# Kernel tuning notes

Hardware: AMD Instinct MI355X
Metric: run time of the kernel (lower is better)

Reference implementation:

```python
import jax, jax.numpy as jnp
import numpy as np

NUM_HEADS = 16

def setup_inputs() -> dict:
    key = jax.random.key(0)
    ks = jax.random.split(key, 7)
    B, N, D = 2, 2048, 1024
    x = jax.random.normal(ks[0], (B, N, D), dtype=jnp.float32)
    gamma = jax.random.uniform(ks[1], (B, NUM_HEADS), dtype=jnp.float32)
    dist_matrix = jax.random.uniform(ks[2], (N, N), dtype=jnp.float32)
    W_qkv = jax.random.normal(ks[3], (D, 3 * D), dtype=jnp.float32) * (D ** -0.5)
    b_qkv = jnp.zeros((3 * D,), dtype=jnp.float32)
    W_proj = jax.random.normal(ks[4], (D, D), dtype=jnp.float32) * (D ** -0.5)
    b_proj = jnp.zeros((D,), dtype=jnp.float32)
    return {"x": x, "gamma": gamma, "dist_matrix": dist_matrix,
            "W_qkv": W_qkv, "b_qkv": b_qkv, "W_proj": W_proj, "b_proj": b_proj}

def reference(x, gamma, dist_matrix, W_qkv, b_qkv, W_proj, b_proj):
    B, N, D = x.shape
    H = NUM_HEADS
    hd = D // H
    scale = D ** -0.5  # standard_scale=False -> dim**-0.5
    # qkv projection: [B,N,3D] -> [3,B,H,N,hd]
    qkv = (x @ W_qkv + b_qkv).reshape(B, N, 3, H, hd).transpose(2, 0, 3, 1, 4)
    q, k, v = qkv[0], qkv[1], qkv[2]
    # scores with zoom bias: [B,H,N,N]
    scores = jnp.einsum('bhnd,bhmd->bhnm', q, k) * scale
    scores = scores - gamma[:, :, None, None] * dist_matrix[None, None, :, :]
    attn = jax.nn.softmax(scores, axis=-1)
    out = jnp.einsum('bhnm,bhmd->bhnd', attn, v)  # [B,H,N,hd]
    out = out.transpose(0, 2, 1, 3).reshape(B, N, D)
    return out @ W_proj + b_proj
```

## Files before the change

### kernel.cpp

```cpp
#include <hip/hip_runtime.h>
#include <cstdint>
#include <cstddef>

#define HD 64
#define NH 16
#define BATCH 2
#define SEQ 2048
#define DIM 1024
#define SCALE 0.03125f
#define LOG2E 1.4426950408889634f
#define QSCALE (SCALE * LOG2E)
#define NT (SEQ / 64)
#define SOFF 16.0f

typedef short bf16x8 __attribute__((ext_vector_type(8)));
typedef float f32x4 __attribute__((ext_vector_type(4)));
typedef unsigned u32x2 __attribute__((ext_vector_type(2)));
typedef unsigned u32x4 __attribute__((ext_vector_type(4)));

#define GL16(gp, lp) __builtin_amdgcn_global_load_lds( \
    (const __attribute__((address_space(1))) unsigned int*)(gp), \
    (__attribute__((address_space(3))) unsigned int*)(lp), 16, 0, 0)

static __device__ __forceinline__ unsigned short f2bf(float f) {
  union { float f; unsigned u; } a; a.f = f;
  unsigned r = a.u + 0x7fffu + ((a.u >> 16) & 1u);
  return (unsigned short)(r >> 16);
}

static __device__ __forceinline__ f32x4 zero4() {
  f32x4 z; z[0] = 0.f; z[1] = 0.f; z[2] = 0.f; z[3] = 0.f; return z;
}

__global__ void convert_x(const float* __restrict__ in, unsigned short* __restrict__ out, int n4) {
  int i = blockIdx.x * blockDim.x + threadIdx.x;
  if (i < n4) {
    float4 v = reinterpret_cast<const float4*>(in)[i];
    ushort4 o;
    o.x = f2bf(v.x); o.y = f2bf(v.y); o.z = f2bf(v.z); o.w = f2bf(v.w);
    reinterpret_cast<ushort4*>(out)[i] = o;
  }
}

__global__ void transpose_convert(const float* __restrict__ in, unsigned short* __restrict__ out,
                                  int R, int C) {
  __shared__ float tile[32][33];
  int bx = blockIdx.x * 32;
  int by = blockIdx.y * 32;
  int tx = threadIdx.x, ty = threadIdx.y;
  #pragma unroll
  for (int i = 0; i < 32; i += 8)
    tile[ty + i][tx] = in[(size_t)(by + ty + i) * C + bx + tx];
  __syncthreads();
  #pragma unroll
  for (int i = 0; i < 32; i += 8)
    out[(size_t)(bx + ty + i) * R + by + tx] = f2bf(tile[tx][ty + i]);
}

__global__ __launch_bounds__(256) void gemm128(
    const unsigned short* __restrict__ A, const unsigned short* __restrict__ Bt,
    const float* __restrict__ bias, int K, int mode,
    unsigned short* __restrict__ qo, unsigned short* __restrict__ ko,
    unsigned short* __restrict__ vo, float* __restrict__ outf) {
  __shared__ __attribute__((aligned(16))) unsigned short As[128 * 64];
  __shared__ __attribute__((aligned(16))) unsigned short Bs[128 * 64];
  const int tid = threadIdx.x;
  const int lane = tid & 63, w = tid >> 6;
  const int lo = lane & 15, hi = lane >> 4;
  const int wm = w >> 1, wn = w & 1;
  const int gx = gridDim.x;
  const int nwg = gx * gridDim.y;
  const int flat = blockIdx.y * gx + blockIdx.x;
  const int swz = (flat & 7) * (nwg >> 3) + (flat >> 3);
  const int m0 = (swz / gx) * 128, n0 = (swz % gx) * 128;
  const int srow = tid >> 3, scol = (tid & 7) * 8;
  const unsigned short* abase = A + (size_t)(m0 + srow) * K + scol;
  const unsigned short* bbase = Bt + (size_t)(n0 + srow) * K + scol;

  f32x4 acc[4][4];
  #pragma unroll
  for (int mr = 0; mr < 4; ++mr)
    #pragma unroll
    for (int nr = 0; nr < 4; ++nr) acc[mr][nr] = zero4();

  const int nkt = K / 64;
  for (int kt = 0; kt < nkt; ++kt) {
    const unsigned short* ak = abase + kt * 64;
    const unsigned short* bk = bbase + kt * 64;
    #pragma unroll
    for (int i = 0; i < 4; ++i) {
      GL16(ak + (size_t)(32 * i) * K, &As[(w * 64 + 256 * i) * 8]);
      GL16(bk + (size_t)(32 * i) * K, &Bs[(w * 64 + 256 * i) * 8]);
    }
    __syncthreads();
    __builtin_amdgcn_s_setprio(1);
    #pragma unroll
    for (int kc = 0; kc < 2; ++kc) {
      bf16x8 af[4], bfr[4];
      #pragma unroll
      for (int mr = 0; mr < 4; ++mr)
        af[mr] = *reinterpret_cast<const bf16x8*>(
            &As[(wm * 64 + mr * 16 + lo) * 64 + kc * 32 + hi * 8]);
      #pragma unroll
      for (int nr = 0; nr < 4; ++nr)
        bfr[nr] = *reinterpret_cast<const bf16x8*>(
            &Bs[(wn * 64 + nr * 16 + lo) * 64 + kc * 32 + hi * 8]);
      #pragma unroll
      for (int mr = 0; mr < 4; ++mr)
        #pragma unroll
        for (int nr = 0; nr < 4; ++nr)
          acc[mr][nr] = __builtin_amdgcn_mfma_f32_16x16x32_bf16(af[mr], bfr[nr], acc[mr][nr], 0, 0, 0);
    }
    __builtin_amdgcn_s_setprio(0);
    __syncthreads();
  }

  #pragma unroll
  for (int nr = 0; nr < 4; ++nr) {
    const int gcol = n0 + wn * 64 + nr * 16 + lo;
    const float bv = bias[gcol];
    #pragma unroll
    for (int mr = 0; mr < 4; ++mr)
      #pragma unroll
      for (int j = 0; j < 4; ++j) {
        const int grow = m0 + wm * 64 + mr * 16 + hi * 4 + j;
        float val = acc[mr][nr][j] + bv;
        if (mode == 0) {
          int which = gcol >> 10;
          int hh = (gcol >> 6) & 15;
          int d = gcol & 63;
          int bb = grow >> 11;
          int n = grow & 2047;
          if (which == 0) {
            qo[((size_t)(bb * NH + hh) * SEQ + n) * HD + d] = f2bf(val * QSCALE);
          } else if (which == 1) {
            ko[((size_t)(bb * NH + hh) * SEQ + n) * HD + d] = f2bf(val);
          } else {
            vo[((size_t)(bb * NH + hh) * HD + d) * SEQ + n] = f2bf(val);
          }
        } else {
          outf[(size_t)grow * DIM + gcol] = val;
        }
      }
  }
}

__global__ __launch_bounds__(256, 4) void attn_kernel(
    const unsigned short* __restrict__ qb, const unsigned short* __restrict__ kb,
    const unsigned short* __restrict__ vtb, const float* __restrict__ gamma,
    const float* __restrict__ dist, unsigned short* __restrict__ ab) {
  __shared__ __attribute__((aligned(16))) unsigned short Ks[2][64 * 64];
  __shared__ __attribute__((aligned(16))) unsigned short Vt[2][64 * 64];
  __shared__ __attribute__((aligned(16))) unsigned short Ps[4 * 16 * 64];
  const int tid = threadIdx.x;
  const int lane = tid & 63;
  const int w = tid >> 6;
  const int lo = lane & 15;
  const int hi = lane >> 4;
  const int idx = blockIdx.x;
  const int bh = idx & 31;
  const int qt = idx >> 5;
  const int b = bh >> 4, h = bh & 15;
  const int qrow0 = qt * 64 + w * 16;
  const float g2 = gamma[bh] * LOG2E;

  const size_t base = (size_t)bh * SEQ * HD;
  const size_t vtbase = (size_t)bh * HD * SEQ;

  bf16x8 qf[2];
  #pragma unroll
  for (int kc = 0; kc < 2; ++kc)
    qf[kc] = *reinterpret_cast<const bf16x8*>(
        &qb[base + (size_t)(qrow0 + lo) * HD + kc * 32 + hi * 8]);

  const float* drow = dist + (size_t)(qrow0 + lo) * SEQ + hi * 4;

  f32x4 o[4];
  #pragma unroll
  for (int db = 0; db < 4; ++db) o[db] = zero4();
  float l_run = 0.f;

  const int srow = tid >> 3;
  const int schunk = (tid & 7) ^ (srow & 7);
  const unsigned short* ksrc0 = kb + base + (size_t)srow * HD + schunk * 8;
  const unsigned short* ksrc1 = ksrc0 + (size_t)32 * HD;
  const unsigned short* vsrc0 = vtb + vtbase + (size_t)srow * SEQ + schunk * 8;
  const unsigned short* vsrc1 = vsrc0 + (size_t)32 * SEQ;

  unsigned short* const psw = &Ps[w * 1024 + lo * 64];

  GL16(ksrc0, &Ks[0][w * 512]);
  GL16(ksrc1, &Ks[0][2048 + w * 512]);
  GL16(vsrc0, &Vt[0][w * 512]);
  GL16(vsrc1, &Vt[0][2048 + w * 512]);

#define ITER(T, CUR)                                                                   \
  {                                                                                    \
                                \
    asm volatile("s_waitcnt vmcnt(2)" ::: "memory");                                   \
    __builtin_amdgcn_s_barrier();                                                      \
                      \
    f32x4 dv[4];                                                                       \
    { const float* dp = drow + (T) * 64;                                               \
      _Pragma("unroll")                                                                \
      for (int nb = 0; nb < 4; ++nb)                                                   \
        dv[nb] = *reinterpret_cast<const f32x4*>(dp + nb * 16);                        \
    }                                                                                  \
    __builtin_amdgcn_sched_barrier(0);                                                 \
                                                                  \
    if ((T) + 1 < NT) {                                                                \
      const size_t m1 = (size_t)((T) + 1) * 64;                                        \
      GL16(ksrc0 + m1 * HD, &Ks[(CUR) ^ 1][w * 512]);                                  \
      GL16(ksrc1 + m1 * HD, &Ks[(CUR) ^ 1][2048 + w * 512]);                           \
    }                                                                                  \
    __builtin_amdgcn_sched_barrier(0);                                                 \
                                                         \
    f32x4 s[4];                                                                        \
    _Pragma("unroll")                                                                  \
    for (int nb = 0; nb < 4; ++nb) {                                                   \
      s[nb][0] = -SOFF; s[nb][1] = -SOFF; s[nb][2] = -SOFF; s[nb][3] = -SOFF;          \
    }                                                                                  \
    __builtin_amdgcn_s_setprio(1);                                                     \
    _Pragma("unroll")                                                                  \
    for (int nb = 0; nb < 4; ++nb)                                                     \
      _Pragma("unroll")                                                                \
      for (int kc = 0; kc < 2; ++kc) {                                                 \
        bf16x8 kf = *reinterpret_cast<const bf16x8*>(                                  \
            &Ks[CUR][(nb * 16 + lo) * 64 + ((kc * 4 + hi) ^ (lo & 7)) * 8]);           \
        s[nb] = __builtin_amdgcn_mfma_f32_16x16x32_bf16(kf, qf[kc], s[nb], 0, 0, 0);   \
      }                                                                                \
    __builtin_amdgcn_s_setprio(0);                                                     \
                         \
    float psum = 0.f;                                                                  \
    _Pragma("unroll")                                                                  \
    for (int nb = 0; nb < 4; ++nb) {                                                   \
      float p0 = exp2f(__builtin_fmaf(-g2, dv[nb][0], s[nb][0]));                      \
      float p1 = exp2f(__builtin_fmaf(-g2, dv[nb][1], s[nb][1]));                      \
      float p2 = exp2f(__builtin_fmaf(-g2, dv[nb][2], s[nb][2]));                      \
      float p3 = exp2f(__builtin_fmaf(-g2, dv[nb][3], s[nb][3]));                      \
      psum += (p0 + p1) + (p2 + p3);                                                   \
      unsigned pk0, pk1;                                                               \
      asm("v_cvt_pk_bf16_f32 %0, %1, %2" : "=v"(pk0) : "v"(p0), "v"(p1));              \
      asm("v_cvt_pk_bf16_f32 %0, %1, %2" : "=v"(pk1) : "v"(p2), "v"(p3));              \
      u32x2 pw_; pw_[0] = pk0; pw_[1] = pk1;                                           \
      *reinterpret_cast<u32x2*>(&psw[(((nb << 2) + hi) ^ lo) * 4]) = pw_;              \
    }                                                                                  \
    psum += __shfl_xor(psum, 16, 64);                                                  \
    psum += __shfl_xor(psum, 32, 64);                                                  \
    l_run += psum;                                                                     \
                  \
    if ((T) + 1 < NT)                                                                  \
      asm volatile("s_waitcnt vmcnt(2)" ::: "memory");                                 \
    else                                                                               \
      asm volatile("s_waitcnt vmcnt(0)" ::: "memory");                                 \
    __builtin_amdgcn_s_barrier();                                                      \
                                                                  \
    if ((T) + 1 < NT) {                                                                \
      const int m1 = ((T) + 1) * 64;                                                   \
      GL16(vsrc0 + m1, &Vt[(CUR) ^ 1][w * 512]);                                       \
      GL16(vsrc1 + m1, &Vt[(CUR) ^ 1][2048 + w * 512]);                                \
    }                                                                                  \
    __builtin_amdgcn_sched_barrier(0);                                                 \
                                  \
    __builtin_amdgcn_s_setprio(1);                                                     \
    _Pragma("unroll")                                                                  \
    for (int kc = 0; kc < 2; ++kc) {                                                   \
      u32x2 ra = *reinterpret_cast<const u32x2*>(&psw[(((kc << 3) + hi * 2) ^ lo) * 4]); \
      u32x2 rb = *reinterpret_cast<const u32x2*>(&psw[(((kc << 3) + hi * 2 + 1) ^ lo) * 4]); \
      u32x4 t_; t_[0] = ra[0]; t_[1] = ra[1]; t_[2] = rb[0]; t_[3] = rb[1];            \
      bf16x8 pf = __builtin_bit_cast(bf16x8, t_);                                      \
      _Pragma("unroll")                                                                \
      for (int db = 0; db < 4; ++db) {                                                 \
        bf16x8 vtf = *reinterpret_cast<const bf16x8*>(                                 \
            &Vt[CUR][(db * 16 + lo) * 64 + ((kc * 4 + hi) ^ (lo & 7)) * 8]);           \
        o[db] = __builtin_amdgcn_mfma_f32_16x16x32_bf16(vtf, pf, o[db], 0, 0, 0);      \
      }                                                                                \
    }                                                                                  \
    __builtin_amdgcn_s_setprio(0);                                                     \
  }

  for (int mt = 0; mt < NT; mt += 2) {
    ITER(mt, 0)
    ITER(mt + 1, 1)
  }
#undef ITER

  {
    float rl = 1.0f / l_run;
    size_t row = (size_t)b * SEQ + qrow0 + lo;
    #pragma unroll
    for (int db = 0; db < 4; ++db) {
      ushort4 w4;
      w4.x = f2bf(o[db][0] * rl);
      w4.y = f2bf(o[db][1] * rl);
      w4.z = f2bf(o[db][2] * rl);
      w4.w = f2bf(o[db][3] * rl);
      *reinterpret_cast<ushort4*>(&ab[row * DIM + h * HD + db * 16 + hi * 4]) = w4;
    }
  }
}

extern "C" void kernel_launch(void* const* d_in, const int* in_sizes, int n_in,
                              void* d_out, int out_size, void* d_ws, size_t ws_size,
                              hipStream_t stream) {
  const float* x     = (const float*)d_in[0];
  const float* gamma = (const float*)d_in[1];
  const float* dist  = (const float*)d_in[2];
  const float* Wqkv  = (const float*)d_in[3];
  const float* bqkv  = (const float*)d_in[4];
  const float* Wproj = (const float*)d_in[5];
  const float* bproj = (const float*)d_in[6];
  float* out = (float*)d_out;

  char* ws = (char*)d_ws;
  unsigned short* xb     = (unsigned short*)(ws);
  unsigned short* wqkvt  = (unsigned short*)(ws + 8388608);
  unsigned short* wprojt = (unsigned short*)(ws + 14680064);
  unsigned short* qbuf   = (unsigned short*)(ws + 16777216);
  unsigned short* kbuf   = (unsigned short*)(ws + 25165824);
  unsigned short* vtbuf  = (unsigned short*)(ws + 33554432);
  unsigned short* abuf   = (unsigned short*)(ws + 41943040);

  convert_x<<<4096, 256, 0, stream>>>(x, xb, (BATCH * SEQ * DIM) / 4);
  transpose_convert<<<dim3(96, 32), dim3(32, 8), 0, stream>>>(Wqkv, wqkvt, DIM, 3 * DIM);
  transpose_convert<<<dim3(32, 32), dim3(32, 8), 0, stream>>>(Wproj, wprojt, DIM, DIM);
  gemm128<<<dim3(24, 32), 256, 0, stream>>>(xb, wqkvt, bqkv, DIM, 0, qbuf, kbuf, vtbuf, nullptr);
  attn_kernel<<<(SEQ / 64) * BATCH * NH, 256, 0, stream>>>(qbuf, kbuf, vtbuf, gamma, dist, abuf);
  gemm128<<<dim3(8, 32), 256, 0, stream>>>(abuf, wprojt, bproj, DIM, 1, nullptr, nullptr, nullptr, out);
}
```

Baseline: 170.8 us.

## Split attention KV range in halves with a separate combine kernel

Adds a split-KV attention path in which each block processes one 1024-key half, using 32-key tiles with smaller LDS buffers and launch bounds of 8 blocks per SM, and writes unnormalized partial outputs and row sums in fp32. A combine kernel then sums the two halves, normalizes, and writes bf16 in the layout the projection GEMM expects. The aim is to double the block count (2048 instead of 1024) and raise occupancy on the many-CU GPU. The cost is extra fp32 partial traffic to global memory, one more kernel launch, and smaller tiles that do less MFMA work per barrier. The path only runs when the workspace is large enough; otherwise the old kernel is used.

New measurement: 334.7 us. +96.0%, slower.

```diff
diff --git a/kernel.cpp b/kernel.cpp
--- a/kernel.cpp
+++ b/kernel.cpp
@@ -11,6 +11,7 @@
 #define LOG2E 1.4426950408889634f
 #define QSCALE (SCALE * LOG2E)
 #define NT (SEQ / 64)
+#define NT2 32
 #define SOFF 16.0f
 
 typedef short bf16x8 __attribute__((ext_vector_type(8)));
@@ -145,6 +146,164 @@
   }
 }
 
+__global__ __launch_bounds__(256, 8) void attn_split(
+    const unsigned short* __restrict__ qb, const unsigned short* __restrict__ kb,
+    const unsigned short* __restrict__ vtb, const float* __restrict__ gamma,
+    const float* __restrict__ dist, float* __restrict__ oP, float* __restrict__ lP) {
+  __shared__ __attribute__((aligned(16))) unsigned short Ks[2][32 * 64];
+  __shared__ __attribute__((aligned(16))) unsigned short Vt[2][64 * 32];
+  __shared__ __attribute__((aligned(16))) unsigned short Ps[4 * 16 * 32];
+  const int tid = threadIdx.x;
+  const int lane = tid & 63;
+  const int w = tid >> 6;
+  const int lo = lane & 15;
+  const int hi = lane >> 4;
+  const int idx = blockIdx.x;
+  const int half = idx & 1;
+  const int bh = (idx >> 1) & 31;
+  const int qt = idx >> 6;
+  const int qrow0 = qt * 64 + w * 16;
+  const int kv0 = half * 1024;
+  const float g2 = gamma[bh] * LOG2E;
+
+  const size_t base = (size_t)bh * SEQ * HD;
+  const size_t vtbase = (size_t)bh * HD * SEQ;
+
+  bf16x8 qf[2];
+  #pragma unroll
+  for (int kc = 0; kc < 2; ++kc)
+    qf[kc] = *reinterpret_cast<const bf16x8*>(
+        &qb[base + (size_t)(qrow0 + lo) * HD + kc * 32 + hi * 8]);
+
+  const float* drow = dist + (size_t)(qrow0 + lo) * SEQ + kv0 + hi * 4;
+
+  f32x4 o[4];
+  #pragma unroll
+  for (int db = 0; db < 4; ++db) o[db] = zero4();
+  float l_run = 0.f;
+
+  const int ksr = tid >> 3;
+  const int ksc = (tid & 7) ^ (ksr & 7);
+  const unsigned short* ksrc = kb + base + (size_t)(kv0 + ksr) * HD + ksc * 8;
+  const int vsr = tid >> 2;
+  const int vsc = (tid & 3) ^ ((vsr >> 1) & 3);
+  const unsigned short* vsrc = vtb + vtbase + (size_t)vsr * SEQ + kv0 + vsc * 8;
+
+  unsigned short* const psw = &Ps[w * 512 + lo * 32];
+
+  GL16(ksrc, &Ks[0][w * 512]);
+  GL16(vsrc, &Vt[0][w * 512]);
+
+#define SITER(T, CUR)                                                                  \
+  {                                                                                    \
+                                              \
+    asm volatile("s_waitcnt vmcnt(1)" ::: "memory");                                   \
+    __builtin_amdgcn_s_barrier();                                                      \
+          \
+    f32x4 dv[2];                                                                       \
+    { const float* dp = drow + (T) * 32;                                               \
+      dv[0] = *reinterpret_cast<const f32x4*>(dp);                                     \
+      dv[1] = *reinterpret_cast<const f32x4*>(dp + 16);                                \
+    }                                                                                  \
+    __builtin_amdgcn_sched_barrier(0);                                                 \
+    if ((T) + 1 < NT2) {                                                               \
+      GL16(ksrc + (size_t)((T) + 1) * 32 * HD, &Ks[(CUR) ^ 1][w * 512]);               \
+    }                                                                                  \
+    __builtin_amdgcn_sched_barrier(0);                                                 \
+                                                            \
+    f32x4 s[2];                                                                        \
+    s[0][0] = -SOFF; s[0][1] = -SOFF; s[0][2] = -SOFF; s[0][3] = -SOFF;                \
+    s[1] = s[0];                                                                       \
+    __builtin_amdgcn_s_setprio(1);                                                     \
+    _Pragma("unroll")                                                                  \
+    for (int nb = 0; nb < 2; ++nb)                                                     \
+      _Pragma("unroll")                                                                \
+      for (int kc = 0; kc < 2; ++kc) {                                                 \
+        bf16x8 kf = *reinterpret_cast<const bf16x8*>(                                  \
+            &Ks[CUR][(nb * 16 + lo) * 64 + ((kc * 4 + hi) ^ (lo & 7)) * 8]);           \
+        s[nb] = __builtin_amdgcn_mfma_f32_16x16x32_bf16(kf, qf[kc], s[nb], 0, 0, 0);   \
+      }                                                                                \
+    __builtin_amdgcn_s_setprio(0);                                                     \
+                \
+    float psum = 0.f;                                                                  \
+    _Pragma("unroll")                                                                  \
+    for (int nb = 0; nb < 2; ++nb) {                                                   \
+      float p0 = exp2f(__builtin_fmaf(-g2, dv[nb][0], s[nb][0]));                      \
+      float p1 = exp2f(__builtin_fmaf(-g2, dv[nb][1], s[nb][1]));                      \
+      float p2 = exp2f(__builtin_fmaf(-g2, dv[nb][2], s[nb][2]));                      \
+      float p3 = exp2f(__builtin_fmaf(-g2, dv[nb][3], s[nb][3]));                      \
+      psum += (p0 + p1) + (p2 + p3);                                                   \
+      unsigned pk0, pk1;                                                               \
+      asm("v_cvt_pk_bf16_f32 %0, %1, %2" : "=v"(pk0) : "v"(p0), "v"(p1));              \
+      asm("v_cvt_pk_bf16_f32 %0, %1, %2" : "=v"(pk1) : "v"(p2), "v"(p3));              \
+      u32x2 pw_; pw_[0] = pk0; pw_[1] = pk1;                                           \
+      *reinterpret_cast<u32x2*>(&psw[((nb * 4 + hi) ^ (lo & 7)) * 4]) = pw_;           \
+    }                                                                                  \
+    psum += __shfl_xor(psum, 16, 64);                                                  \
+    psum += __shfl_xor(psum, 32, 64);                                                  \
+    l_run += psum;                                                                     \
+                                  \
+    if ((T) + 1 < NT2)                                                                 \
+      asm volatile("s_waitcnt vmcnt(1)" ::: "memory");                                 \
+    else                                                                               \
+      asm volatile("s_waitcnt vmcnt(0)" ::: "memory");                                 \
+    __builtin_amdgcn_s_barrier();                                                      \
+    if ((T) + 1 < NT2) {                                                               \
+      GL16(vsrc + ((T) + 1) * 32, &Vt[(CUR) ^ 1][w * 512]);                            \
+    }                                                                                  \
+    __builtin_amdgcn_sched_barrier(0);                                                 \
+                                               \
+    __builtin_amdgcn_s_setprio(1);                                                     \
+    {                                                                                  \
+      u32x2 ra = *reinterpret_cast<const u32x2*>(&psw[((hi * 2) ^ (lo & 7)) * 4]);     \
+      u32x2 rb = *reinterpret_cast<const u32x2*>(&psw[((hi * 2 + 1) ^ (lo & 7)) * 4]); \
+      u32x4 t_; t_[0] = ra[0]; t_[1] = ra[1]; t_[2] = rb[0]; t_[3] = rb[1];            \
+      bf16x8 pf = __builtin_bit_cast(bf16x8, t_);                                      \
+      _Pragma("unroll")                                                                \
+      for (int db = 0; db < 4; ++db) {                                                 \
+        bf16x8 vtf = *reinterpret_cast<const bf16x8*>(                                 \
+            &Vt[CUR][(db * 16 + lo) * 32 + ((hi ^ ((lo >> 1) & 3))) * 8]);             \
+        o[db] = __builtin_amdgcn_mfma_f32_16x16x32_bf16(vtf, pf, o[db], 0, 0, 0);      \
+      }                                                                                \
+    }                                                                                  \
+    __builtin_amdgcn_s_setprio(0);                                                     \
+  }
+
+  for (int mt = 0; mt < NT2; mt += 2) {
+    SITER(mt, 0)
+    SITER(mt + 1, 1)
+  }
+#undef SITER
+
+  {
+    const size_t prow = (size_t)(half * 32 + bh) * SEQ + qrow0 + lo;
+    float* op = oP + prow * HD + hi * 4;
+    #pragma unroll
+    for (int db = 0; db < 4; ++db)
+      *reinterpret_cast<f32x4*>(op + db * 16) = o[db];
+    if (hi == 0) lP[prow] = l_run;
+  }
+}
+
+__global__ __launch_bounds__(256) void attn_combine(
+    const float* __restrict__ oP, const float* __restrict__ lP,
+    unsigned short* __restrict__ ab) {
+  int g = blockIdx.x * blockDim.x + threadIdx.x;
+  int row = g >> 4;
+  int dc = (g & 15) * 4;
+  int bh = row >> 11, n = row & 2047;
+  int b = bh >> 4, h = bh & 15;
+  f32x4 a = *reinterpret_cast<const f32x4*>(oP + (size_t)row * 64 + dc);
+  f32x4 c = *reinterpret_cast<const f32x4*>(oP + 4194304 + (size_t)row * 64 + dc);
+  float rl = 1.0f / (lP[row] + lP[65536 + row]);
+  ushort4 w4;
+  w4.x = f2bf((a[0] + c[0]) * rl);
+  w4.y = f2bf((a[1] + c[1]) * rl);
+  w4.z = f2bf((a[2] + c[2]) * rl);
+  w4.w = f2bf((a[3] + c[3]) * rl);
+  *reinterpret_cast<ushort4*>(&ab[((size_t)(b * SEQ + n)) * DIM + h * HD + dc]) = w4;
+}
+
 __global__ __launch_bounds__(256, 4) void attn_kernel(
     const unsigned short* __restrict__ qb, const unsigned short* __restrict__ kb,
     const unsigned short* __restrict__ vtb, const float* __restrict__ gamma,
@@ -196,10 +355,8 @@
 
 #define ITER(T, CUR)                                                                   \
   {                                                                                    \
-                                \
     asm volatile("s_waitcnt vmcnt(2)" ::: "memory");                                   \
     __builtin_amdgcn_s_barrier();                                                      \
-                      \
     f32x4 dv[4];                                                                       \
     { const float* dp = drow + (T) * 64;                                               \
       _Pragma("unroll")                                                                \
@@ -207,14 +364,12 @@
         dv[nb] = *reinterpret_cast<const f32x4*>(dp + nb * 16);                        \
     }                                                                                  \
     __builtin_amdgcn_sched_barrier(0);                                                 \
-                                                                  \
     if ((T) + 1 < NT) {                                                                \
       const size_t m1 = (size_t)((T) + 1) * 64;                                        \
       GL16(ksrc0 + m1 * HD, &Ks[(CUR) ^ 1][w * 512]);                                  \
       GL16(ksrc1 + m1 * HD, &Ks[(CUR) ^ 1][2048 + w * 512]);                           \
     }                                                                                  \
     __builtin_amdgcn_sched_barrier(0);                                                 \
-                                                         \
     f32x4 s[4];                                                                        \
     _Pragma("unroll")                                                                  \
     for (int nb = 0; nb < 4; ++nb) {                                                   \
@@ -230,7 +385,6 @@
         s[nb] = __builtin_amdgcn_mfma_f32_16x16x32_bf16(kf, qf[kc], s[nb], 0, 0, 0);   \
       }                                                                                \
     __builtin_amdgcn_s_setprio(0);                                                     \
-                         \
     float psum = 0.f;                                                                  \
     _Pragma("unroll")                                                                  \
     for (int nb = 0; nb < 4; ++nb) {                                                   \
@@ -248,20 +402,17 @@
     psum += __shfl_xor(psum, 16, 64);                                                  \
     psum += __shfl_xor(psum, 32, 64);                                                  \
     l_run += psum;                                                                     \
-                  \
     if ((T) + 1 < NT)                                                                  \
       asm volatile("s_waitcnt vmcnt(2)" ::: "memory");                                 \
     else                                                                               \
       asm volatile("s_waitcnt vmcnt(0)" ::: "memory");                                 \
     __builtin_amdgcn_s_barrier();                                                      \
-                                                                  \
     if ((T) + 1 < NT) {                                                                \
       const int m1 = ((T) + 1) * 64;                                                   \
       GL16(vsrc0 + m1, &Vt[(CUR) ^ 1][w * 512]);                                       \
       GL16(vsrc1 + m1, &Vt[(CUR) ^ 1][2048 + w * 512]);                                \
     }                                                                                  \
     __builtin_amdgcn_sched_barrier(0);                                                 \
-                                  \
     __builtin_amdgcn_s_setprio(1);                                                     \
     _Pragma("unroll")                                                                  \
     for (int kc = 0; kc < 2; ++kc) {                                                   \
@@ -320,11 +471,19 @@
   unsigned short* kbuf   = (unsigned short*)(ws + 25165824);
   unsigned short* vtbuf  = (unsigned short*)(ws + 33554432);
   unsigned short* abuf   = (unsigned short*)(ws + 41943040);
+  float* oP = (float*)(ws + 50331648);
+  float* lP = (float*)(ws + 83886080);
+  const bool split = ws_size >= (size_t)84410368;
 
   convert_x<<<4096, 256, 0, stream>>>(x, xb, (BATCH * SEQ * DIM) / 4);
   transpose_convert<<<dim3(96, 32), dim3(32, 8), 0, stream>>>(Wqkv, wqkvt, DIM, 3 * DIM);
   transpose_convert<<<dim3(32, 32), dim3(32, 8), 0, stream>>>(Wproj, wprojt, DIM, DIM);
   gemm128<<<dim3(24, 32), 256, 0, stream>>>(xb, wqkvt, bqkv, DIM, 0, qbuf, kbuf, vtbuf, nullptr);
-  attn_kernel<<<(SEQ / 64) * BATCH * NH, 256, 0, stream>>>(qbuf, kbuf, vtbuf, gamma, dist, abuf);
+  if (split) {
+    attn_split<<<2048, 256, 0, stream>>>(qbuf, kbuf, vtbuf, gamma, dist, oP, lP);
+    attn_combine<<<4096, 256, 0, stream>>>(oP, lP, abuf);
+  } else {
+    attn_kernel<<<(SEQ / 64) * BATCH * NH, 256, 0, stream>>>(qbuf, kbuf, vtbuf, gamma, dist, abuf);
+  }
   gemm128<<<dim3(8, 32), 256, 0, stream>>>(abuf, wprojt, bproj, DIM, 1, nullptr, nullptr, nullptr, out);
 }
```
